# Kernel tuning notes

Measured on AMD Instinct MI355X. Metric: run time of the kernel, lower is better.

The kernel has to match this reference:

```python
import jax, jax.numpy as jnp
import numpy as np

N_NODES = 50000
IN_F = 256
OUT_F = 128
N_EDGES = 800000

def setup_inputs() -> dict:
    key = jax.random.key(0)
    k1, k2, k3, k4, k5 = jax.random.split(key, 5)
    x = jax.random.normal(k1, (N_NODES, IN_F), dtype=jnp.float32)
    # xavier_uniform on [in, out]
    limit = float(np.sqrt(6.0 / (IN_F + OUT_F)))
    weight = jax.random.uniform(k2, (IN_F, OUT_F), dtype=jnp.float32, minval=-limit, maxval=limit)
    adj_vals = jax.random.uniform(k3, (N_EDGES,), dtype=jnp.float32)
    adj_rows = jax.random.randint(k4, (N_EDGES,), 0, N_NODES, dtype=jnp.int32)
    adj_cols = jax.random.randint(k5, (N_EDGES,), 0, N_NODES, dtype=jnp.int32)
    return {"x": x, "weight": weight, "adj_vals": adj_vals, "adj_rows": adj_rows, "adj_cols": adj_cols}

def reference(x, weight, adj_vals, adj_rows, adj_cols):
    # dropout p=0.0 (eval) is identity
    support = x @ weight                      # [N, out]
    msgs = adj_vals[:, None] * support[adj_cols]  # [E, out] gather + scale
    output = jax.ops.segment_sum(msgs, adj_rows, num_segments=N_NODES)  # spmm
    return jax.nn.relu(output)
```

## Files before the change

kernel.cpp:

```cpp
#include <hip/hip_runtime.h>
#include <hip/hip_bf16.h>


#define IN_F  256
#define OUT_F 128

#define BM 64
#define BK 32
#define KP 40

typedef __attribute__((ext_vector_type(8))) short s16x8;
typedef __attribute__((ext_vector_type(4))) float f32x4;

static __device__ __forceinline__ unsigned short f2bf(float f) {
    union { float f; unsigned u; } v; v.f = f;
    unsigned r = v.u + 0x7FFFu + ((v.u >> 16) & 1u);
    return (unsigned short)(r >> 16);
}
static __device__ __forceinline__ float bf2f(unsigned short b) {
    union { unsigned u; float f; } v; v.u = ((unsigned)b) << 16;
    return v.f;
}

__global__ __launch_bounds__(256) void gcn_wsplit_kernel(
    const float* __restrict__ w, unsigned short* __restrict__ wh_T,
    unsigned short* __restrict__ wl_T)
{
    int cell = blockIdx.x * 256 + threadIdx.x;
    int c  = cell & (OUT_F - 1);
    int kq = cell >> 7;
    unsigned short h[4], l[4];
#pragma unroll
    for (int d = 0; d < 4; ++d) {
        float f = w[(size_t)(kq * 4 + d) * OUT_F + c];
        h[d] = f2bf(f);
        l[d] = f2bf(f - bf2f(h[d]));
    }
    *reinterpret_cast<ushort4*>(&wh_T[(size_t)c * IN_F + kq * 4]) =
        make_ushort4(h[0], h[1], h[2], h[3]);
    *reinterpret_cast<ushort4*>(&wl_T[(size_t)c * IN_F + kq * 4]) =
        make_ushort4(l[0], l[1], l[2], l[3]);
}

__global__ __launch_bounds__(256) void gcn_gemm_mfma_kernel(
    const float* __restrict__ x,
    const unsigned short* __restrict__ wh_T,
    const unsigned short* __restrict__ wl_T,
    unsigned short* __restrict__ support_bf, int n_nodes)
{
    __shared__ unsigned short xh_lds[BM][KP];
    __shared__ unsigned short xl_lds[BM][KP];
    __shared__ unsigned short wh_lds[OUT_F][KP];
    __shared__ unsigned short wl_lds[OUT_F][KP];

    const int tid  = threadIdx.x;
    const int lane = tid & 63;
    const int wid  = tid >> 6;
    const int wm   = (wid >> 1) * 32;
    const int wn   = (wid & 1) * 64;
    const int row0 = blockIdx.x * BM;

    const int lr = lane & 15;
    const int lg = lane >> 4;

    f32x4 acc[2][4];
#pragma unroll
    for (int st = 0; st < 2; ++st)
#pragma unroll
        for (int nt = 0; nt < 4; ++nt)
            acc[st][nt] = (f32x4){0.f, 0.f, 0.f, 0.f};

    for (int k0 = 0; k0 < IN_F; k0 += BK) {
        if (k0 > 0) __syncthreads();

#pragma unroll
        for (int i = 0; i < 2; ++i) {
            int cell = i * 256 + tid;
            int r    = cell >> 3;
            int kq   = cell & 7;
            int row  = row0 + r;
            float4 xv = make_float4(0.f, 0.f, 0.f, 0.f);
            if (row < n_nodes)
                xv = *reinterpret_cast<const float4*>(
                    &x[(size_t)row * IN_F + k0 + kq * 4]);
            unsigned short h0 = f2bf(xv.x), h1 = f2bf(xv.y),
                           h2 = f2bf(xv.z), h3 = f2bf(xv.w);
            *reinterpret_cast<ushort4*>(&xh_lds[r][kq * 4]) =
                make_ushort4(h0, h1, h2, h3);
            *reinterpret_cast<ushort4*>(&xl_lds[r][kq * 4]) =
                make_ushort4(f2bf(xv.x - bf2f(h0)), f2bf(xv.y - bf2f(h1)),
                             f2bf(xv.z - bf2f(h2)), f2bf(xv.w - bf2f(h3)));
        }
#pragma unroll
        for (int i = 0; i < 2; ++i) {
            int cell = i * 256 + tid;
            int c    = cell >> 2;
            int p    = cell & 3;
            s16x8 hv = *reinterpret_cast<const s16x8*>(
                &wh_T[(size_t)c * IN_F + k0 + p * 8]);
            s16x8 lv = *reinterpret_cast<const s16x8*>(
                &wl_T[(size_t)c * IN_F + k0 + p * 8]);
            *reinterpret_cast<s16x8*>(&wh_lds[c][p * 8]) = hv;
            *reinterpret_cast<s16x8*>(&wl_lds[c][p * 8]) = lv;
        }
        __syncthreads();

        s16x8 ah[2], al[2], bh[4], bl[4];
#pragma unroll
        for (int st = 0; st < 2; ++st) {
            int m = wm + st * 16 + lr;
            ah[st] = *reinterpret_cast<const s16x8*>(&xh_lds[m][lg * 8]);
            al[st] = *reinterpret_cast<const s16x8*>(&xl_lds[m][lg * 8]);
        }
#pragma unroll
        for (int nt = 0; nt < 4; ++nt) {
            int c = wn + nt * 16 + lr;
            bh[nt] = *reinterpret_cast<const s16x8*>(&wh_lds[c][lg * 8]);
            bl[nt] = *reinterpret_cast<const s16x8*>(&wl_lds[c][lg * 8]);
        }

#pragma unroll
        for (int st = 0; st < 2; ++st)
#pragma unroll
            for (int nt = 0; nt < 4; ++nt) {
                acc[st][nt] = __builtin_amdgcn_mfma_f32_16x16x32_bf16(
                    ah[st], bh[nt], acc[st][nt], 0, 0, 0);
                acc[st][nt] = __builtin_amdgcn_mfma_f32_16x16x32_bf16(
                    al[st], bh[nt], acc[st][nt], 0, 0, 0);
                acc[st][nt] = __builtin_amdgcn_mfma_f32_16x16x32_bf16(
                    ah[st], bl[nt], acc[st][nt], 0, 0, 0);
            }
    }

#pragma unroll
    for (int st = 0; st < 2; ++st) {
#pragma unroll
        for (int nt = 0; nt < 4; ++nt) {
#pragma unroll
            for (int r = 0; r < 4; ++r) {
                int m = row0 + wm + st * 16 + lg * 4 + r;
                int n = wn + nt * 16 + lr;
                if (m < n_nodes)
                    support_bf[(size_t)m * OUT_F + n] = f2bf(acc[st][nt][r]);
            }
        }
    }
}

#define VBK 32
#define XPAD 68
__global__ __launch_bounds__(256) void gcn_gemm_valu_kernel(
    const float* __restrict__ x, const float* __restrict__ w,
    float* __restrict__ support, int n_nodes)
{
    __shared__ float xs_t[VBK][XPAD];
    __shared__ float ws_[VBK][OUT_F];

    const int tid  = threadIdx.x;
    const int cg   = tid & 31;
    const int rg   = tid >> 5;
    const int row0 = blockIdx.x * BM;

    float acc[8][4];
#pragma unroll
    for (int i = 0; i < 8; ++i)
#pragma unroll
        for (int j = 0; j < 4; ++j) acc[i][j] = 0.f;

    for (int k0 = 0; k0 < IN_F; k0 += VBK) {
        if (k0 > 0) __syncthreads();
#pragma unroll
        for (int i = 0; i < 2; ++i) {
            int t   = tid + i * 256;
            int r   = t >> 3;
            int kk  = (t & 7) << 2;
            int row = row0 + r;
            float4 v = make_float4(0.f, 0.f, 0.f, 0.f);
            if (row < n_nodes)
                v = *reinterpret_cast<const float4*>(&x[(size_t)row * IN_F + k0 + kk]);
            xs_t[kk + 0][r] = v.x;
            xs_t[kk + 1][r] = v.y;
            xs_t[kk + 2][r] = v.z;
            xs_t[kk + 3][r] = v.w;
        }
#pragma unroll
        for (int i = 0; i < 4; ++i) {
            int fi = tid + i * 256;
            int kk = fi >> 5;
            int cc = (fi & 31) << 2;
            *reinterpret_cast<float4*>(&ws_[kk][cc]) =
                *reinterpret_cast<const float4*>(&w[(size_t)(k0 + kk) * OUT_F + cc]);
        }
        __syncthreads();
#pragma unroll
        for (int kk = 0; kk < VBK; ++kk) {
            float4 a0 = *reinterpret_cast<const float4*>(&xs_t[kk][rg * 4]);
            float4 a1 = *reinterpret_cast<const float4*>(&xs_t[kk][rg * 4 + 32]);
            float4 b  = *reinterpret_cast<const float4*>(&ws_[kk][cg * 4]);
            const float av[8] = {a0.x, a0.y, a0.z, a0.w, a1.x, a1.y, a1.z, a1.w};
            const float bv[4] = {b.x, b.y, b.z, b.w};
#pragma unroll
            for (int i = 0; i < 8; ++i)
#pragma unroll
                for (int j = 0; j < 4; ++j)
                    acc[i][j] += av[i] * bv[j];
        }
    }
#pragma unroll
    for (int i = 0; i < 8; ++i) {
        int row = row0 + rg * 4 + (i & 3) + (i >> 2) * 32;
        if (row < n_nodes) {
            float4 o = make_float4(acc[i][0], acc[i][1], acc[i][2], acc[i][3]);
            *reinterpret_cast<float4*>(&support[(size_t)row * OUT_F + cg * 4]) = o;
        }
    }
}

__global__ __launch_bounds__(256) void gcn_hist_kernel(
    const int* __restrict__ rows, int* __restrict__ deg, int n_edges)
{
    int e = blockIdx.x * blockDim.x + threadIdx.x;
    if (e < n_edges) atomicAdd(&deg[rows[e]], 1);
}

__global__ __launch_bounds__(256) void gcn_scan1_kernel(
    const int* __restrict__ deg, int* __restrict__ offsets,
    int* __restrict__ block_sums, int n)
{
    __shared__ int part[256];
    const int tid  = threadIdx.x;
    const int base = blockIdx.x * 1024 + tid * 4;

    int4 v = make_int4(0, 0, 0, 0);
    if (base + 3 < n) {
        v = *reinterpret_cast<const int4*>(&deg[base]);
    } else {
        if (base + 0 < n) v.x = deg[base + 0];
        if (base + 1 < n) v.y = deg[base + 1];
        if (base + 2 < n) v.z = deg[base + 2];
        if (base + 3 < n) v.w = deg[base + 3];
    }
    int s = v.x + v.y + v.z + v.w;
    part[tid] = s;
    __syncthreads();
    for (int d = 1; d < 256; d <<= 1) {
        int t = (tid >= d) ? part[tid - d] : 0;
        __syncthreads();
        part[tid] += t;
        __syncthreads();
    }
    int ex = part[tid] - s;
    int4 o;
    o.x = ex;
    o.y = o.x + v.x;
    o.z = o.y + v.y;
    o.w = o.z + v.z;
    if (base + 3 < n) {
        *reinterpret_cast<int4*>(&offsets[base]) = o;
    } else {
        if (base + 0 < n) offsets[base + 0] = o.x;
        if (base + 1 < n) offsets[base + 1] = o.y;
        if (base + 2 < n) offsets[base + 2] = o.z;
        if (base + 3 < n) offsets[base + 3] = o.w;
    }
    if (tid == 255) block_sums[blockIdx.x] = part[255];
}

__global__ __launch_bounds__(256) void gcn_scan2_kernel(
    int* __restrict__ block_sums, int nb)
{
    __shared__ int part[256];
    const int tid = threadIdx.x;
    int s = (tid < nb) ? block_sums[tid] : 0;
    part[tid] = s;
    __syncthreads();
    for (int d = 1; d < 256; d <<= 1) {
        int t = (tid >= d) ? part[tid - d] : 0;
        __syncthreads();
        part[tid] += t;
        __syncthreads();
    }
    if (tid < nb) block_sums[tid] = part[tid] - s;
}

__global__ __launch_bounds__(256) void gcn_scan3_kernel(
    int* __restrict__ offsets, const int* __restrict__ block_sums, int n)
{
    const int base = blockIdx.x * 1024 + threadIdx.x * 4;
    const int add  = block_sums[blockIdx.x];
    if (base + 3 < n) {
        int4 v = *reinterpret_cast<const int4*>(&offsets[base]);
        v.x += add; v.y += add; v.z += add; v.w += add;
        *reinterpret_cast<int4*>(&offsets[base]) = v;
    } else {
        if (base + 0 < n) offsets[base + 0] += add;
        if (base + 1 < n) offsets[base + 1] += add;
        if (base + 2 < n) offsets[base + 2] += add;
        if (base + 3 < n) offsets[base + 3] += add;
    }
}

__global__ __launch_bounds__(256) void gcn_fill_kernel(
    const int* __restrict__ rows, const int* __restrict__ cols,
    const float* __restrict__ vals, int* __restrict__ offsets,
    unsigned int* __restrict__ csr_cv, int n_edges)
{
    int e = blockIdx.x * blockDim.x + threadIdx.x;
    if (e >= n_edges) return;
    int r = rows[e];
    int pos = atomicAdd(&offsets[r], 1);
    unsigned int cv = ((unsigned int)f2bf(vals[e]) << 16) | (unsigned int)cols[e];
    __builtin_nontemporal_store(cv, &csr_cv[pos]);
}

__global__ __launch_bounds__(256) void gcn_gather_kernel(
    const unsigned short* __restrict__ support_bf,
    const int* __restrict__ offsets,
    const unsigned int* __restrict__ csr_cv,
    float* __restrict__ out, int n_nodes)
{
    const int node = blockIdx.x * 4 + (threadIdx.x >> 6);
    const int lane = threadIdx.x & 63;
    if (node >= n_nodes) return;

    const int end   = offsets[node];
    const int start = (node == 0) ? 0 : offsets[node - 1];
    const int d     = end - start;
    const int off   = start;

    float2 acc = make_float2(0.f, 0.f);
    int j = 0;
    for (; j + 3 < d; j += 4) {
        unsigned int cv0 = csr_cv[off + j];
        unsigned int cv1 = csr_cv[off + j + 1];
        unsigned int cv2 = csr_cv[off + j + 2];
        unsigned int cv3 = csr_cv[off + j + 3];
        ushort2 s0 = *reinterpret_cast<const ushort2*>(
            &support_bf[(size_t)(cv0 & 0xFFFFu) * OUT_F + lane * 2]);
        ushort2 s1 = *reinterpret_cast<const ushort2*>(
            &support_bf[(size_t)(cv1 & 0xFFFFu) * OUT_F + lane * 2]);
        ushort2 s2 = *reinterpret_cast<const ushort2*>(
            &support_bf[(size_t)(cv2 & 0xFFFFu) * OUT_F + lane * 2]);
        ushort2 s3 = *reinterpret_cast<const ushort2*>(
            &support_bf[(size_t)(cv3 & 0xFFFFu) * OUT_F + lane * 2]);
        float v0 = bf2f((unsigned short)(cv0 >> 16));
        float v1 = bf2f((unsigned short)(cv1 >> 16));
        float v2 = bf2f((unsigned short)(cv2 >> 16));
        float v3 = bf2f((unsigned short)(cv3 >> 16));
        acc.x += v0 * bf2f(s0.x) + v1 * bf2f(s1.x) + v2 * bf2f(s2.x) + v3 * bf2f(s3.x);
        acc.y += v0 * bf2f(s0.y) + v1 * bf2f(s1.y) + v2 * bf2f(s2.y) + v3 * bf2f(s3.y);
    }
    for (; j < d; ++j) {
        unsigned int cv0 = csr_cv[off + j];
        ushort2 s0 = *reinterpret_cast<const ushort2*>(
            &support_bf[(size_t)(cv0 & 0xFFFFu) * OUT_F + lane * 2]);
        float v0 = bf2f((unsigned short)(cv0 >> 16));
        acc.x += v0 * bf2f(s0.x);
        acc.y += v0 * bf2f(s0.y);
    }

    float2 o;
    o.x = fmaxf(acc.x, 0.f);
    o.y = fmaxf(acc.y, 0.f);
    *reinterpret_cast<float2*>(&out[(size_t)node * OUT_F + lane * 2]) = o;
}

__global__ __launch_bounds__(256) void gcn_scatter_kernel(
    const float* __restrict__ support, const float* __restrict__ vals,
    const int* __restrict__ rows, const int* __restrict__ cols,
    float* __restrict__ out, int n_edges)
{
    long long idx   = (long long)blockIdx.x * blockDim.x + threadIdx.x;
    long long total = (long long)n_edges * (OUT_F / 4);
    if (idx >= total) return;

    int e  = (int)(idx >> 5);
    int f4 = (int)(idx & 31);
    int r  = rows[e];
    int c  = cols[e];
    float v = vals[e];

    float4 s = *reinterpret_cast<const float4*>(&support[(size_t)c * OUT_F + f4 * 4]);
    float* o = &out[(size_t)r * OUT_F + f4 * 4];
    atomicAdd(o + 0, v * s.x);
    atomicAdd(o + 1, v * s.y);
    atomicAdd(o + 2, v * s.z);
    atomicAdd(o + 3, v * s.w);
}

__global__ __launch_bounds__(256) void gcn_relu_kernel(float* __restrict__ out, int n4)
{
    int idx = blockIdx.x * blockDim.x + threadIdx.x;
    if (idx >= n4) return;
    float4* p = reinterpret_cast<float4*>(out) + idx;
    float4 v = *p;
    v.x = fmaxf(v.x, 0.f);
    v.y = fmaxf(v.y, 0.f);
    v.z = fmaxf(v.z, 0.f);
    v.w = fmaxf(v.w, 0.f);
    *p = v;
}

static inline char* align16(char* p) {
    return (char*)(((uintptr_t)p + 15) & ~(uintptr_t)15);
}

extern "C" void kernel_launch(void* const* d_in, const int* in_sizes, int n_in,
                              void* d_out, int out_size, void* d_ws, size_t ws_size,
                              hipStream_t stream)
{
    const float* x    = (const float*)d_in[0];
    const float* w    = (const float*)d_in[1];
    const float* vals = (const float*)d_in[2];
    const int*   rows = (const int*)d_in[3];
    const int*   cols = (const int*)d_in[4];
    float* out = (float*)d_out;

    const int n_nodes = in_sizes[0] / IN_F;
    const int n_edges = in_sizes[2];

    const int scan_blocks = (n_nodes + 1023) / 1024;

    char* p = (char*)d_ws;
    char*           supp_raw = p;                 p = align16(p + (size_t)n_nodes * OUT_F * sizeof(float));
    unsigned short* wh_T    = (unsigned short*)p; p = align16(p + (size_t)OUT_F * IN_F * sizeof(short));
    unsigned short* wl_T    = (unsigned short*)p; p = align16(p + (size_t)OUT_F * IN_F * sizeof(short));
    int*            offsets = (int*)p;            p = align16(p + (size_t)n_nodes * sizeof(int));
    int*            deg     = (int*)p;            p = align16(p + (size_t)n_nodes * sizeof(int));
    int*            bsums   = (int*)p;            p = align16(p + (size_t)256 * sizeof(int));
    unsigned int*   csr_cv  = (unsigned int*)p;   p = align16(p + (size_t)n_edges * sizeof(unsigned int));
    size_t needed = (size_t)(p - (char*)d_ws);

    const int gemm_blocks = (n_nodes + BM - 1) / BM;
    const int eb = (n_edges + 255) / 256;

    if (ws_size >= needed && scan_blocks <= 256 && n_nodes <= 65536) {
        unsigned short* support_bf = (unsigned short*)supp_raw;
        gcn_wsplit_kernel<<<(OUT_F * IN_F / 4) / 256, 256, 0, stream>>>(w, wh_T, wl_T);
        gcn_gemm_mfma_kernel<<<gemm_blocks, 256, 0, stream>>>(x, wh_T, wl_T,
                                                              support_bf, n_nodes);
        hipMemsetAsync(deg, 0, (size_t)n_nodes * sizeof(int), stream);
        gcn_hist_kernel<<<eb, 256, 0, stream>>>(rows, deg, n_edges);
        gcn_scan1_kernel<<<scan_blocks, 256, 0, stream>>>(deg, offsets, bsums, n_nodes);
        gcn_scan2_kernel<<<1, 256, 0, stream>>>(bsums, scan_blocks);
        gcn_scan3_kernel<<<scan_blocks, 256, 0, stream>>>(offsets, bsums, n_nodes);
        gcn_fill_kernel<<<eb, 256, 0, stream>>>(rows, cols, vals, offsets,
                                                csr_cv, n_edges);
        int gb = (n_nodes + 3) / 4;
        gcn_gather_kernel<<<gb, 256, 0, stream>>>(support_bf, offsets,
                                                  csr_cv, out, n_nodes);
    } else {
        float* support = (float*)supp_raw;
        gcn_gemm_valu_kernel<<<gemm_blocks, 256, 0, stream>>>(x, w, support, n_nodes);
        hipMemsetAsync(d_out, 0, (size_t)out_size * sizeof(float), stream);
        long long total = (long long)n_edges * (OUT_F / 4);
        int sc_blocks = (int)((total + 255) / 256);
        gcn_scatter_kernel<<<sc_blocks, 256, 0, stream>>>(support, vals, rows, cols,
                                                          out, n_edges);
        int n4 = out_size / 4;
        gcn_relu_kernel<<<(n4 + 255) / 256, 256, 0, stream>>>(out, n4);
    }
}
```

Measured before the change: 160.5 us.

## Partition CSR build into per-XCD edge ranges with separate offset arrays

Edges are split into 8 contiguous partitions, each with its own degree histogram and offset array, so key space becomes partition×node. Blocks are swizzled so consecutive hardware block slots (likely mapped to different XCDs) each handle one partition, aiming to keep atomics for histogram and fill local to one die's cache. The scan now handles 8x more keys with 8 elements per thread, and the gather iterates over 8 per-node segments with smaller unroll, adding loop and offset-load overhead.

```diff
diff --git a/kernel.cpp b/kernel.cpp
--- a/kernel.cpp
+++ b/kernel.cpp
@@ -4,6 +4,7 @@
 
 #define IN_F  256
 #define OUT_F 128
+#define NPART 8
 
 #define BM 64
 #define BK 32
@@ -217,10 +218,14 @@
 }
 
 __global__ __launch_bounds__(256) void gcn_hist_kernel(
-    const int* __restrict__ rows, int* __restrict__ deg, int n_edges)
-{
-    int e = blockIdx.x * blockDim.x + threadIdx.x;
-    if (e < n_edges) atomicAdd(&deg[rows[e]], 1);
+    const int* __restrict__ rows, int* __restrict__ deg,
+    int n_edges, int n_nodes, int epp, int nb8)
+{
+    int l = (blockIdx.x & 7) * (nb8 >> 3) + (blockIdx.x >> 3);
+    int e = l * 256 + threadIdx.x;
+    if (e >= n_edges) return;
+    int p = e / epp;
+    atomicAdd(&deg[(size_t)p * n_nodes + rows[e]], 1);
 }
 
 __global__ __launch_bounds__(256) void gcn_scan1_kernel(
@@ -229,18 +234,24 @@
 {
     __shared__ int part[256];
     const int tid  = threadIdx.x;
-    const int base = blockIdx.x * 1024 + tid * 4;
-
-    int4 v = make_int4(0, 0, 0, 0);
-    if (base + 3 < n) {
-        v = *reinterpret_cast<const int4*>(&deg[base]);
+    const int base = blockIdx.x * 2048 + tid * 8;
+
+    int v[8];
+#pragma unroll
+    for (int q = 0; q < 8; ++q) v[q] = 0;
+    if (base + 7 < n) {
+        int4 a = *reinterpret_cast<const int4*>(&deg[base]);
+        int4 b = *reinterpret_cast<const int4*>(&deg[base + 4]);
+        v[0] = a.x; v[1] = a.y; v[2] = a.z; v[3] = a.w;
+        v[4] = b.x; v[5] = b.y; v[6] = b.z; v[7] = b.w;
     } else {
-        if (base + 0 < n) v.x = deg[base + 0];
-        if (base + 1 < n) v.y = deg[base + 1];
-        if (base + 2 < n) v.z = deg[base + 2];
-        if (base + 3 < n) v.w = deg[base + 3];
-    }
-    int s = v.x + v.y + v.z + v.w;
+#pragma unroll
+        for (int q = 0; q < 8; ++q)
+            if (base + q < n) v[q] = deg[base + q];
+    }
+    int s = 0;
+#pragma unroll
+    for (int q = 0; q < 8; ++q) s += v[q];
     part[tid] = s;
     __syncthreads();
     for (int d = 1; d < 256; d <<= 1) {
@@ -249,19 +260,17 @@
         part[tid] += t;
         __syncthreads();
     }
-    int ex = part[tid] - s;
-    int4 o;
-    o.x = ex;
-    o.y = o.x + v.x;
-    o.z = o.y + v.y;
-    o.w = o.z + v.z;
-    if (base + 3 < n) {
-        *reinterpret_cast<int4*>(&offsets[base]) = o;
+    int run = part[tid] - s;
+    int o[8];
+#pragma unroll
+    for (int q = 0; q < 8; ++q) { o[q] = run; run += v[q]; }
+    if (base + 7 < n) {
+        *reinterpret_cast<int4*>(&offsets[base])     = make_int4(o[0], o[1], o[2], o[3]);
+        *reinterpret_cast<int4*>(&offsets[base + 4]) = make_int4(o[4], o[5], o[6], o[7]);
     } else {
-        if (base + 0 < n) offsets[base + 0] = o.x;
-        if (base + 1 < n) offsets[base + 1] = o.y;
-        if (base + 2 < n) offsets[base + 2] = o.z;
-        if (base + 3 < n) offsets[base + 3] = o.w;
+#pragma unroll
+        for (int q = 0; q < 8; ++q)
+            if (base + q < n) offsets[base + q] = o[q];
     }
     if (tid == 255) block_sums[blockIdx.x] = part[255];
 }
@@ -286,31 +295,36 @@
 __global__ __launch_bounds__(256) void gcn_scan3_kernel(
     int* __restrict__ offsets, const int* __restrict__ block_sums, int n)
 {
-    const int base = blockIdx.x * 1024 + threadIdx.x * 4;
+    const int base = blockIdx.x * 2048 + threadIdx.x * 8;
     const int add  = block_sums[blockIdx.x];
-    if (base + 3 < n) {
-        int4 v = *reinterpret_cast<const int4*>(&offsets[base]);
-        v.x += add; v.y += add; v.z += add; v.w += add;
-        *reinterpret_cast<int4*>(&offsets[base]) = v;
+    if (base + 7 < n) {
+        int4 a = *reinterpret_cast<const int4*>(&offsets[base]);
+        int4 b = *reinterpret_cast<const int4*>(&offsets[base + 4]);
+        a.x += add; a.y += add; a.z += add; a.w += add;
+        b.x += add; b.y += add; b.z += add; b.w += add;
+        *reinterpret_cast<int4*>(&offsets[base])     = a;
+        *reinterpret_cast<int4*>(&offsets[base + 4]) = b;
     } else {
-        if (base + 0 < n) offsets[base + 0] += add;
-        if (base + 1 < n) offsets[base + 1] += add;
-        if (base + 2 < n) offsets[base + 2] += add;
-        if (base + 3 < n) offsets[base + 3] += add;
+#pragma unroll
+        for (int q = 0; q < 8; ++q)
+            if (base + q < n) offsets[base + q] += add;
     }
 }
 
 __global__ __launch_bounds__(256) void gcn_fill_kernel(
     const int* __restrict__ rows, const int* __restrict__ cols,
     const float* __restrict__ vals, int* __restrict__ offsets,
-    unsigned int* __restrict__ csr_cv, int n_edges)
-{
-    int e = blockIdx.x * blockDim.x + threadIdx.x;
+    unsigned int* __restrict__ csr_cv,
+    int n_edges, int n_nodes, int epp, int nb8)
+{
+    int l = (blockIdx.x & 7) * (nb8 >> 3) + (blockIdx.x >> 3);
+    int e = l * 256 + threadIdx.x;
     if (e >= n_edges) return;
+    int p = e / epp;
     int r = rows[e];
-    int pos = atomicAdd(&offsets[r], 1);
+    int pos = atomicAdd(&offsets[(size_t)p * n_nodes + r], 1);
     unsigned int cv = ((unsigned int)f2bf(vals[e]) << 16) | (unsigned int)cols[e];
-    __builtin_nontemporal_store(cv, &csr_cv[pos]);
+    csr_cv[pos] = cv;
 }
 
 __global__ __launch_bounds__(256) void gcn_gather_kernel(
@@ -323,40 +337,33 @@
     const int lane = threadIdx.x & 63;
     if (node >= n_nodes) return;
 
-    const int end   = offsets[node];
-    const int start = (node == 0) ? 0 : offsets[node - 1];
-    const int d     = end - start;
-    const int off   = start;
-
     float2 acc = make_float2(0.f, 0.f);
-    int j = 0;
-    for (; j + 3 < d; j += 4) {
-        unsigned int cv0 = csr_cv[off + j];
-        unsigned int cv1 = csr_cv[off + j + 1];
-        unsigned int cv2 = csr_cv[off + j + 2];
-        unsigned int cv3 = csr_cv[off + j + 3];
-        ushort2 s0 = *reinterpret_cast<const ushort2*>(
-            &support_bf[(size_t)(cv0 & 0xFFFFu) * OUT_F + lane * 2]);
-        ushort2 s1 = *reinterpret_cast<const ushort2*>(
-            &support_bf[(size_t)(cv1 & 0xFFFFu) * OUT_F + lane * 2]);
-        ushort2 s2 = *reinterpret_cast<const ushort2*>(
-            &support_bf[(size_t)(cv2 & 0xFFFFu) * OUT_F + lane * 2]);
-        ushort2 s3 = *reinterpret_cast<const ushort2*>(
-            &support_bf[(size_t)(cv3 & 0xFFFFu) * OUT_F + lane * 2]);
-        float v0 = bf2f((unsigned short)(cv0 >> 16));
-        float v1 = bf2f((unsigned short)(cv1 >> 16));
-        float v2 = bf2f((unsigned short)(cv2 >> 16));
-        float v3 = bf2f((unsigned short)(cv3 >> 16));
-        acc.x += v0 * bf2f(s0.x) + v1 * bf2f(s1.x) + v2 * bf2f(s2.x) + v3 * bf2f(s3.x);
-        acc.y += v0 * bf2f(s0.y) + v1 * bf2f(s1.y) + v2 * bf2f(s2.y) + v3 * bf2f(s3.y);
-    }
-    for (; j < d; ++j) {
-        unsigned int cv0 = csr_cv[off + j];
-        ushort2 s0 = *reinterpret_cast<const ushort2*>(
-            &support_bf[(size_t)(cv0 & 0xFFFFu) * OUT_F + lane * 2]);
-        float v0 = bf2f((unsigned short)(cv0 >> 16));
-        acc.x += v0 * bf2f(s0.x);
-        acc.y += v0 * bf2f(s0.y);
+#pragma unroll
+    for (int p = 0; p < NPART; ++p) {
+        const int i     = p * n_nodes + node;
+        const int start = (i == 0) ? 0 : offsets[i - 1];
+        const int end   = offsets[i];
+        int j = start;
+        for (; j + 1 < end; j += 2) {
+            unsigned int cv0 = csr_cv[j];
+            unsigned int cv1 = csr_cv[j + 1];
+            ushort2 s0 = *reinterpret_cast<const ushort2*>(
+                &support_bf[(size_t)(cv0 & 0xFFFFu) * OUT_F + lane * 2]);
+            ushort2 s1 = *reinterpret_cast<const ushort2*>(
+                &support_bf[(size_t)(cv1 & 0xFFFFu) * OUT_F + lane * 2]);
+            float v0 = bf2f((unsigned short)(cv0 >> 16));
+            float v1 = bf2f((unsigned short)(cv1 >> 16));
+            acc.x += v0 * bf2f(s0.x) + v1 * bf2f(s1.x);
+            acc.y += v0 * bf2f(s0.y) + v1 * bf2f(s1.y);
+        }
+        if (j < end) {
+            unsigned int cv0 = csr_cv[j];
+            ushort2 s0 = *reinterpret_cast<const ushort2*>(
+                &support_bf[(size_t)(cv0 & 0xFFFFu) * OUT_F + lane * 2]);
+            float v0 = bf2f((unsigned short)(cv0 >> 16));
+            acc.x += v0 * bf2f(s0.x);
+            acc.y += v0 * bf2f(s0.y);
+        }
     }
 
     float2 o;
@@ -419,33 +426,36 @@
     const int n_nodes = in_sizes[0] / IN_F;
     const int n_edges = in_sizes[2];
 
-    const int scan_blocks = (n_nodes + 1023) / 1024;
+    const int n_keys      = NPART * n_nodes;
+    const int scan_blocks = (n_keys + 2047) / 2048;
+    const int epp         = (n_edges + NPART - 1) / NPART;
 
     char* p = (char*)d_ws;
     char*           supp_raw = p;                 p = align16(p + (size_t)n_nodes * OUT_F * sizeof(float));
     unsigned short* wh_T    = (unsigned short*)p; p = align16(p + (size_t)OUT_F * IN_F * sizeof(short));
     unsigned short* wl_T    = (unsigned short*)p; p = align16(p + (size_t)OUT_F * IN_F * sizeof(short));
-    int*            offsets = (int*)p;            p = align16(p + (size_t)n_nodes * sizeof(int));
-    int*            deg     = (int*)p;            p = align16(p + (size_t)n_nodes * sizeof(int));
+    int*            offsets = (int*)p;            p = align16(p + (size_t)n_keys * sizeof(int));
+    int*            deg     = (int*)p;            p = align16(p + (size_t)n_keys * sizeof(int));
     int*            bsums   = (int*)p;            p = align16(p + (size_t)256 * sizeof(int));
     unsigned int*   csr_cv  = (unsigned int*)p;   p = align16(p + (size_t)n_edges * sizeof(unsigned int));
     size_t needed = (size_t)(p - (char*)d_ws);
 
     const int gemm_blocks = (n_nodes + BM - 1) / BM;
-    const int eb = (n_edges + 255) / 256;
+    const int eb  = (n_edges + 255) / 256;
+    const int nb8 = ((eb + 7) / 8) * 8;
 
     if (ws_size >= needed && scan_blocks <= 256 && n_nodes <= 65536) {
         unsigned short* support_bf = (unsigned short*)supp_raw;
         gcn_wsplit_kernel<<<(OUT_F * IN_F / 4) / 256, 256, 0, stream>>>(w, wh_T, wl_T);
         gcn_gemm_mfma_kernel<<<gemm_blocks, 256, 0, stream>>>(x, wh_T, wl_T,
                                                               support_bf, n_nodes);
-        hipMemsetAsync(deg, 0, (size_t)n_nodes * sizeof(int), stream);
-        gcn_hist_kernel<<<eb, 256, 0, stream>>>(rows, deg, n_edges);
-        gcn_scan1_kernel<<<scan_blocks, 256, 0, stream>>>(deg, offsets, bsums, n_nodes);
+        hipMemsetAsync(deg, 0, (size_t)n_keys * sizeof(int), stream);
+        gcn_hist_kernel<<<nb8, 256, 0, stream>>>(rows, deg, n_edges, n_nodes, epp, nb8);
+        gcn_scan1_kernel<<<scan_blocks, 256, 0, stream>>>(deg, offsets, bsums, n_keys);
         gcn_scan2_kernel<<<1, 256, 0, stream>>>(bsums, scan_blocks);
-        gcn_scan3_kernel<<<scan_blocks, 256, 0, stream>>>(offsets, bsums, n_nodes);
-        gcn_fill_kernel<<<eb, 256, 0, stream>>>(rows, cols, vals, offsets,
-                                                csr_cv, n_edges);
+        gcn_scan3_kernel<<<scan_blocks, 256, 0, stream>>>(offsets, bsums, n_keys);
+        gcn_fill_kernel<<<nb8, 256, 0, stream>>>(rows, cols, vals, offsets,
+                                                 csr_cv, n_edges, n_nodes, epp, nb8);
         int gb = (n_nodes + 3) / 4;
         gcn_gather_kernel<<<gb, 256, 0, stream>>>(support_bf, offsets,
                                                   csr_cv, out, n_nodes);
```

Measured after the change: 181.5 us. 1.13x slower.
